# Optimization experiments

Measured on AMD Instinct MI355X. Metric: run time of the kernel, lower is better.

Reference implementation:

```python
import jax, jax.numpy as jnp
import numpy as np

B, T, H, N = 4, 2048, 1024, 16
DT_MIN, DT_MAX = 1e-3, 1e-1
A_INIT_MIN, A_INIT_MAX = 0.5, 2.0


def _inv_softplus(x):
    # log(exp(x) - 1), numerically stable
    return x + jnp.log(-jnp.expm1(-x))


def setup_inputs() -> dict:
    key = jax.random.key(0)
    kx, ka, kb, kc, kw, kdt = jax.random.split(key, 6)
    x = jax.random.normal(kx, (B, T, H), dtype=jnp.float32)
    A_log = jax.random.uniform(ka, (H, N), minval=np.log(A_INIT_MIN), maxval=np.log(A_INIT_MAX), dtype=jnp.float32)
    B_mat = 0.02 * jax.random.normal(kb, (H, N), dtype=jnp.float32)
    C_mat = 0.02 * jax.random.normal(kc, (H, N), dtype=jnp.float32)
    D_vec = jnp.ones((H,), dtype=jnp.float32)
    W_dt = 0.02 * jax.random.normal(kw, (H, H), dtype=jnp.float32)
    b_dt = _inv_softplus(jax.random.uniform(kdt, (H,), minval=DT_MIN, maxval=DT_MAX, dtype=jnp.float32))
    return {"x": x, "A_log": A_log, "B_mat": B_mat, "C_mat": C_mat, "D_vec": D_vec, "W_dt": W_dt, "b_dt": b_dt}


def reference(x, A_log, B_mat, C_mat, D_vec, W_dt, b_dt):
    # in_proj is Identity since input_size == hidden_size
    u = x  # (B, T, H)
    A = -jnp.exp(A_log)  # (H, N)
    # dt for all timesteps at once: softplus(u @ W_dt^T + b_dt) -> (B, T, H)
    dt = jax.nn.softplus(jnp.einsum('bth,gh->btg', u, W_dt) + b_dt)
    state0 = jnp.zeros((u.shape[0], A_log.shape[0], A_log.shape[1]), dtype=u.dtype)

    def step(state, inp):
        dt_t, u_t = inp  # (B, H), (B, H)
        dtA = dt_t[..., None]  # (B, H, 1)
        A_bar = jnp.exp(dtA * A)                       # (B, H, N)
        state = A_bar * state + (dtA * B_mat) * u_t[..., None]
        y_t = jnp.einsum('bhn,hn->bh', state, C_mat) + D_vec * u_t
        return state, y_t

    # scan over time axis
    state_final, ys = jax.lax.scan(step, state0, (dt.transpose(1, 0, 2), u.transpose(1, 0, 2)))
    out = ys.transpose(1, 0, 2)  # (B, T, H)
    return out, state_final
```

## Files before the change

kernel.cpp:

```cpp
#include <hip/hip_runtime.h>
#include <stdint.h>

#define BB 4
#define TT 2048
#define HH 1024
#define NN 16
#define KK 1024
#define GG 1024
#define MM (BB*TT)
#define NCHUNK 64
#define TC (TT/NCHUNK)
#define HB 256

#if __has_builtin(__builtin_amdgcn_exp2f)
#define FAST_EXP2(x) __builtin_amdgcn_exp2f(x)
#else
#define FAST_EXP2(x) __expf((x) * 0.6931471805599453f)
#endif
#define EXPSCALE 1.4426950408889634f

typedef __attribute__((ext_vector_type(8))) short short8;
typedef __attribute__((ext_vector_type(4))) float f32x4;

__device__ __forceinline__ unsigned short f2bf(float f) {
  union { float f; unsigned u; } a; a.f = f;
  unsigned u = a.u;
  u += 0x7fffu + ((u >> 16) & 1u);
  return (unsigned short)(u >> 16);
}

__global__ __launch_bounds__(256) void cvt_f32_bf16(const float* __restrict__ src,
                                                    unsigned short* __restrict__ dst, int n4) {
  int i = blockIdx.x * blockDim.x + threadIdx.x;
  if (i >= n4) return;
  float4 a = ((const float4*)src)[i];
  ushort4 o;
  o.x = f2bf(a.x); o.y = f2bf(a.y); o.z = f2bf(a.z); o.w = f2bf(a.w);
  ((ushort4*)dst)[i] = o;
}

__global__ __launch_bounds__(256) void gemm_dt(const unsigned short* __restrict__ xb,
                                               const unsigned short* __restrict__ wb,
                                               const float* __restrict__ b_dt,
                                               float* __restrict__ dtT) {
  __shared__ short lsA[128 * 32];
  __shared__ short lsB[64 * 32];
  const int tid  = threadIdx.x;
  const int w    = tid >> 6;
  const int lane = tid & 63;
  const int m0 = blockIdx.x * 128;
  const int g0 = blockIdx.y * 64;

  const int ea  = w * 1024 + lane * 8;
  const int am0 = ea >> 5,         ak0 = ea & 31;
  const int am1 = (ea + 512) >> 5, ak1 = (ea + 512) & 31;
  const int eb  = w * 512 + lane * 8;
  const int bg0 = eb >> 5,         bk0 = eb & 31;
  const unsigned short* gA0 = xb + (size_t)(m0 + am0) * KK + ak0;
  const unsigned short* gA1 = xb + (size_t)(m0 + am1) * KK + ak1;
  const unsigned short* gB0 = wb + (size_t)(g0 + bg0) * KK + bk0;
  short* lA0 = lsA + w * 1024;
  short* lB0 = lsB + w * 512;

  const int wm   = (w >> 1) * 64;
  const int wg   = (w & 1) * 32;
  const int lrow = lane & 15;
  const int lq   = lane >> 4;

  f32x4 acc[4][2];
  const f32x4 zero = {0.f, 0.f, 0.f, 0.f};
#pragma unroll
  for (int i = 0; i < 4; ++i)
#pragma unroll
    for (int j = 0; j < 2; ++j) acc[i][j] = zero;

  for (int kt = 0; kt < KK / 32; ++kt) {
    const int ko = kt * 32;
    __builtin_amdgcn_global_load_lds((__attribute__((address_space(1))) void*)(gA0 + ko),
                                     (__attribute__((address_space(3))) void*)(lA0), 16, 0, 0);
    __builtin_amdgcn_global_load_lds((__attribute__((address_space(1))) void*)(gA1 + ko),
                                     (__attribute__((address_space(3))) void*)(lA0 + 512), 16, 0, 0);
    __builtin_amdgcn_global_load_lds((__attribute__((address_space(1))) void*)(gB0 + ko),
                                     (__attribute__((address_space(3))) void*)(lB0), 16, 0, 0);
    __syncthreads();

    short8 af[4], bfr[2];
#pragma unroll
    for (int mi = 0; mi < 4; ++mi)
      af[mi] = *(const short8*)&lsA[(wm + mi * 16 + lrow) * 32 + lq * 8];
#pragma unroll
    for (int ni = 0; ni < 2; ++ni)
      bfr[ni] = *(const short8*)&lsB[(wg + ni * 16 + lrow) * 32 + lq * 8];
#pragma unroll
    for (int mi = 0; mi < 4; ++mi)
#pragma unroll
      for (int ni = 0; ni < 2; ++ni)
        acc[mi][ni] = __builtin_amdgcn_mfma_f32_16x16x32_bf16(af[mi], bfr[ni], acc[mi][ni], 0, 0, 0);
    __syncthreads();
  }

  const int b  = m0 >> 11;
  const int tb = (m0 & (TT - 1)) + wm + lq * 4;
#pragma unroll
  for (int mi = 0; mi < 4; ++mi)
#pragma unroll
    for (int ni = 0; ni < 2; ++ni) {
      const int gcol = g0 + wg + ni * 16 + lrow;
      const float bias = b_dt[gcol];
      f32x4 sp;
#pragma unroll
      for (int r = 0; r < 4; ++r) {
        float z = acc[mi][ni][r] + bias;
        sp[r] = fmaxf(z, 0.f) + __logf(1.f + __expf(-fabsf(z)));
      }
      *(f32x4*)&dtT[((size_t)b * HH + gcol) * TT + tb + mi * 16] = sp;
    }
}

__global__ __launch_bounds__(256, 4) void ssm_phase1(const float* __restrict__ x,
                                                     const float* __restrict__ dtT,
                                                     const float* __restrict__ A_log,
                                                     float* __restrict__ sloc,
                                                     float* __restrict__ sdArr) {
  __shared__ float uT[TC][HB];
  const int tid = threadIdx.x;
  const int bid = blockIdx.x;
  const int hb = bid & (HH / HB - 1);
  const int b  = (bid >> 2) & (BB - 1);
  const int c  = bid >> 4;
  const int h  = hb * HB + tid;

  const float* xg = x + (size_t)b * TT * HH + (size_t)c * TC * HH + hb * HB;
#pragma unroll
  for (int i = 0; i < 8; ++i) {
    const int t   = i * 4 + (tid >> 6);
    const int col = (tid & 63) * 4;
    *(f32x4*)&uT[t][col] = *(const f32x4*)&xg[(size_t)t * HH + col];
  }

  const float* dp = dtT + ((size_t)b * HH + h) * TT + c * TC;
  f32x4 dd[8];
#pragma unroll
  for (int i = 0; i < 8; ++i) dd[i] = ((const f32x4*)dp)[i];

  float Ae[NN];
#pragma unroll
  for (int n = 0; n < NN; ++n) Ae[n] = -__expf(A_log[h * NN + n]) * EXPSCALE;

  float s[NN];
#pragma unroll
  for (int n = 0; n < NN; ++n) s[n] = 0.f;
  float sd = 0.f;

  __syncthreads();

#pragma unroll
  for (int jt = 0; jt < 8; ++jt) {
#pragma unroll
    for (int k = 0; k < 4; ++k) {
      const int t = jt * 4 + k;
      const float dtv = dd[jt][k];
      const float du  = dtv * uT[t][tid];
      sd += dtv;
#pragma unroll
      for (int n = 0; n < NN; ++n) {
        const float ab = FAST_EXP2(dtv * Ae[n]);
        s[n] = fmaf(ab, s[n], du);
      }
    }
  }

  float* sp = sloc + (((size_t)c * BB + b) * HH + h) * NN;
#pragma unroll
  for (int n = 0; n < NN; n += 4) {
    f32x4 v = {s[n], s[n + 1], s[n + 2], s[n + 3]};
    *(f32x4*)&sp[n] = v;
  }
  sdArr[((size_t)c * BB + b) * HH + h] = sd;
}

__global__ __launch_bounds__(256) void ssm_phase2(float* __restrict__ sloc,
                                                  const float* __restrict__ sdArr,
                                                  const float* __restrict__ A_log,
                                                  const float* __restrict__ Bm_,
                                                  float* __restrict__ stateOut) {
  const int id = blockIdx.x * 256 + threadIdx.x;
  const int hn = id & (HH * NN - 1);
  const int bh = id >> 4;
  const float Ae = -__expf(A_log[hn]) * EXPSCALE;
  float carry = 0.f;
  for (int ch = 0; ch < NCHUNK; ++ch) {
    const size_t idx = (size_t)ch * (BB * HH * NN) + id;
    const float sl = sloc[idx];
    const float dc = FAST_EXP2(Ae * sdArr[(size_t)ch * (BB * HH) + bh]);
    sloc[idx] = carry;
    carry = fmaf(dc, carry, sl);
  }
  stateOut[id] = Bm_[hn] * carry;
}

__global__ __launch_bounds__(256, 4) void ssm_phase3(const float* __restrict__ x,
                                                     const float* __restrict__ dtT,
                                                     const float* __restrict__ A_log,
                                                     const float* __restrict__ Bm_,
                                                     const float* __restrict__ Cm_,
                                                     const float* __restrict__ Dv_,
                                                     const float* __restrict__ carryBuf,
                                                     float* __restrict__ out) {
  __shared__ float uT[TC][HB];
  const int tid = threadIdx.x;
  const int bid = blockIdx.x;
  const int hb = bid & (HH / HB - 1);
  const int b  = (bid >> 2) & (BB - 1);
  const int c  = bid >> 4;
  const int h  = hb * HB + tid;

  const float* xg = x + (size_t)b * TT * HH + (size_t)c * TC * HH + hb * HB;
#pragma unroll
  for (int i = 0; i < 8; ++i) {
    const int t   = i * 4 + (tid >> 6);
    const int col = (tid & 63) * 4;
    *(f32x4*)&uT[t][col] = *(const f32x4*)&xg[(size_t)t * HH + col];
  }

  const float* dp = dtT + ((size_t)b * HH + h) * TT + c * TC;
  f32x4 dd[8];
#pragma unroll
  for (int i = 0; i < 8; ++i) dd[i] = ((const f32x4*)dp)[i];

  float Ae[NN], Cb[NN];
#pragma unroll
  for (int n = 0; n < NN; ++n) {
    Ae[n] = -__expf(A_log[h * NN + n]) * EXPSCALE;
    Cb[n] = Cm_[h * NN + n] * Bm_[h * NN + n];
  }
  const float Dv = Dv_[h];

  float s[NN];
  const float* cp = carryBuf + (((size_t)c * BB + b) * HH + h) * NN;
#pragma unroll
  for (int n = 0; n < NN; n += 4) {
    f32x4 v = *(const f32x4*)&cp[n];
    s[n] = v[0]; s[n + 1] = v[1]; s[n + 2] = v[2]; s[n + 3] = v[3];
  }

  float* yo = out + (size_t)b * TT * HH + (size_t)c * TC * HH + h;

  __syncthreads();

#pragma unroll
  for (int jt = 0; jt < 8; ++jt) {
#pragma unroll
    for (int k = 0; k < 4; ++k) {
      const int t = jt * 4 + k;
      const float dtv = dd[jt][k];
      const float uv  = uT[t][tid];
      const float du  = dtv * uv;
      float y = Dv * uv;
#pragma unroll
      for (int n = 0; n < NN; ++n) {
        const float ab = FAST_EXP2(dtv * Ae[n]);
        s[n] = fmaf(ab, s[n], du);
        y = fmaf(Cb[n], s[n], y);
      }
      yo[(size_t)t * HH] = y;
    }
  }
}

extern "C" void kernel_launch(void* const* d_in, const int* in_sizes, int n_in,
                              void* d_out, int out_size, void* d_ws, size_t ws_size,
                              hipStream_t stream) {
  const float* x     = (const float*)d_in[0];
  const float* A_log = (const float*)d_in[1];
  const float* B_mat = (const float*)d_in[2];
  const float* C_mat = (const float*)d_in[3];
  const float* D_vec = (const float*)d_in[4];
  const float* W_dt  = (const float*)d_in[5];
  const float* b_dt  = (const float*)d_in[6];
  float* out = (float*)d_out;

  char* ws = (char*)d_ws;
  unsigned short* xb  = (unsigned short*)(ws);
  unsigned short* wb  = (unsigned short*)(ws + 16777216);
  float*          dtT = (float*)(ws + 18874368);
  float*          sloc  = (float*)(ws);
  float*          sdArr = (float*)(ws + 16777216);
  float* stateOut = out + (size_t)BB * TT * HH;

  cvt_f32_bf16<<<(MM * KK / 4 + 255) / 256, 256, 0, stream>>>(x, xb, MM * KK / 4);
  cvt_f32_bf16<<<(GG * KK / 4 + 255) / 256, 256, 0, stream>>>(W_dt, wb, GG * KK / 4);
  gemm_dt<<<dim3(MM / 128, GG / 64), 256, 0, stream>>>(xb, wb, b_dt, dtT);

  const int nblk = (HH / HB) * BB * NCHUNK;
  ssm_phase1<<<nblk, 256, 0, stream>>>(x, dtT, A_log, sloc, sdArr);
  ssm_phase2<<<(BB * HH * NN) / 256, 256, 0, stream>>>(sloc, sdArr, A_log, B_mat, stateOut);
  ssm_phase3<<<nblk, 256, 0, stream>>>(x, dtT, A_log, B_mat, C_mat, D_vec, sloc, out);
}
```

Before: 184.9 us.

## Store dt in fp16, merge conversion launches, use direct-to-LDS loads and split accumulators

The dt intermediate is now written by the GEMM epilogue as fp16 instead of fp32, halving its write and its two reads in the scan phases. The two bf16 conversion launches are merged into one kernel. The x tile is staged into LDS with global_load_lds instead of going through registers. Phase 3 splits the y reduction across four accumulators to shorten the dependency chain, and phase 2 unrolls its chunk loop. fp16 dt loses precision compared with fp32, which feeds directly into the exponent of the decay.

```diff
diff --git a/kernel.cpp b/kernel.cpp
--- a/kernel.cpp
+++ b/kernel.cpp
@@ -21,6 +21,8 @@
 
 typedef __attribute__((ext_vector_type(8))) short short8;
 typedef __attribute__((ext_vector_type(4))) float f32x4;
+typedef __attribute__((ext_vector_type(8))) _Float16 half8;
+typedef __attribute__((ext_vector_type(4))) _Float16 half4;
 
 __device__ __forceinline__ unsigned short f2bf(float f) {
   union { float f; unsigned u; } a; a.f = f;
@@ -29,20 +31,24 @@
   return (unsigned short)(u >> 16);
 }
 
-__global__ __launch_bounds__(256) void cvt_f32_bf16(const float* __restrict__ src,
-                                                    unsigned short* __restrict__ dst, int n4) {
+__global__ __launch_bounds__(256) void cvt2_f32_bf16(const float* __restrict__ srcA,
+                                                     unsigned short* __restrict__ dstA, int n4a,
+                                                     const float* __restrict__ srcB,
+                                                     unsigned short* __restrict__ dstB, int n4b) {
   int i = blockIdx.x * blockDim.x + threadIdx.x;
-  if (i >= n4) return;
-  float4 a = ((const float4*)src)[i];
+  const float* s; unsigned short* d; int j;
+  if (i < n4a) { s = srcA; d = dstA; j = i; }
+  else         { s = srcB; d = dstB; j = i - n4a; if (j >= n4b) return; }
+  float4 a = ((const float4*)s)[j];
   ushort4 o;
   o.x = f2bf(a.x); o.y = f2bf(a.y); o.z = f2bf(a.z); o.w = f2bf(a.w);
-  ((ushort4*)dst)[i] = o;
+  ((ushort4*)d)[j] = o;
 }
 
 __global__ __launch_bounds__(256) void gemm_dt(const unsigned short* __restrict__ xb,
                                                const unsigned short* __restrict__ wb,
                                                const float* __restrict__ b_dt,
-                                               float* __restrict__ dtT) {
+                                               _Float16* __restrict__ dtH) {
   __shared__ short lsA[128 * 32];
   __shared__ short lsB[64 * 32];
   const int tid  = threadIdx.x;
@@ -107,18 +113,18 @@
     for (int ni = 0; ni < 2; ++ni) {
       const int gcol = g0 + wg + ni * 16 + lrow;
       const float bias = b_dt[gcol];
-      f32x4 sp;
+      half4 sp;
 #pragma unroll
       for (int r = 0; r < 4; ++r) {
         float z = acc[mi][ni][r] + bias;
-        sp[r] = fmaxf(z, 0.f) + __logf(1.f + __expf(-fabsf(z)));
+        sp[r] = (_Float16)(fmaxf(z, 0.f) + __logf(1.f + __expf(-fabsf(z))));
       }
-      *(f32x4*)&dtT[((size_t)b * HH + gcol) * TT + tb + mi * 16] = sp;
+      *(half4*)&dtH[((size_t)b * HH + gcol) * TT + tb + mi * 16] = sp;
     }
 }
 
 __global__ __launch_bounds__(256, 4) void ssm_phase1(const float* __restrict__ x,
-                                                     const float* __restrict__ dtT,
+                                                     const _Float16* __restrict__ dtH,
                                                      const float* __restrict__ A_log,
                                                      float* __restrict__ sloc,
                                                      float* __restrict__ sdArr) {
@@ -129,19 +135,27 @@
   const int b  = (bid >> 2) & (BB - 1);
   const int c  = bid >> 4;
   const int h  = hb * HB + tid;
+  const int w    = tid >> 6;
+  const int lane = tid & 63;
 
   const float* xg = x + (size_t)b * TT * HH + (size_t)c * TC * HH + hb * HB;
 #pragma unroll
   for (int i = 0; i < 8; ++i) {
-    const int t   = i * 4 + (tid >> 6);
-    const int col = (tid & 63) * 4;
-    *(f32x4*)&uT[t][col] = *(const f32x4*)&xg[(size_t)t * HH + col];
-  }
-
-  const float* dp = dtT + ((size_t)b * HH + h) * TT + c * TC;
+    const int t = i * 4 + w;
+    __builtin_amdgcn_global_load_lds(
+        (__attribute__((address_space(1))) void*)(xg + (size_t)t * HH + lane * 4),
+        (__attribute__((address_space(3))) void*)&uT[t][0], 16, 0, 0);
+  }
+
+  const _Float16* dp = dtH + ((size_t)b * HH + h) * TT + c * TC;
+  half8 hv[4];
+#pragma unroll
+  for (int i = 0; i < 4; ++i) hv[i] = ((const half8*)dp)[i];
   f32x4 dd[8];
 #pragma unroll
-  for (int i = 0; i < 8; ++i) dd[i] = ((const f32x4*)dp)[i];
+  for (int i = 0; i < 8; ++i)
+#pragma unroll
+    for (int k = 0; k < 4; ++k) dd[i][k] = (float)hv[i >> 1][(i & 1) * 4 + k];
 
   float Ae[NN];
 #pragma unroll
@@ -189,6 +203,7 @@
   const int bh = id >> 4;
   const float Ae = -__expf(A_log[hn]) * EXPSCALE;
   float carry = 0.f;
+#pragma unroll 4
   for (int ch = 0; ch < NCHUNK; ++ch) {
     const size_t idx = (size_t)ch * (BB * HH * NN) + id;
     const float sl = sloc[idx];
@@ -200,7 +215,7 @@
 }
 
 __global__ __launch_bounds__(256, 4) void ssm_phase3(const float* __restrict__ x,
-                                                     const float* __restrict__ dtT,
+                                                     const _Float16* __restrict__ dtH,
                                                      const float* __restrict__ A_log,
                                                      const float* __restrict__ Bm_,
                                                      const float* __restrict__ Cm_,
@@ -214,19 +229,27 @@
   const int b  = (bid >> 2) & (BB - 1);
   const int c  = bid >> 4;
   const int h  = hb * HB + tid;
+  const int w    = tid >> 6;
+  const int lane = tid & 63;
 
   const float* xg = x + (size_t)b * TT * HH + (size_t)c * TC * HH + hb * HB;
 #pragma unroll
   for (int i = 0; i < 8; ++i) {
-    const int t   = i * 4 + (tid >> 6);
-    const int col = (tid & 63) * 4;
-    *(f32x4*)&uT[t][col] = *(const f32x4*)&xg[(size_t)t * HH + col];
-  }
-
-  const float* dp = dtT + ((size_t)b * HH + h) * TT + c * TC;
+    const int t = i * 4 + w;
+    __builtin_amdgcn_global_load_lds(
+        (__attribute__((address_space(1))) void*)(xg + (size_t)t * HH + lane * 4),
+        (__attribute__((address_space(3))) void*)&uT[t][0], 16, 0, 0);
+  }
+
+  const _Float16* dp = dtH + ((size_t)b * HH + h) * TT + c * TC;
+  half8 hv[4];
+#pragma unroll
+  for (int i = 0; i < 4; ++i) hv[i] = ((const half8*)dp)[i];
   f32x4 dd[8];
 #pragma unroll
-  for (int i = 0; i < 8; ++i) dd[i] = ((const f32x4*)dp)[i];
+  for (int i = 0; i < 8; ++i)
+#pragma unroll
+    for (int k = 0; k < 4; ++k) dd[i][k] = (float)hv[i >> 1][(i & 1) * 4 + k];
 
   float Ae[NN], Cb[NN];
 #pragma unroll
@@ -256,14 +279,16 @@
       const float dtv = dd[jt][k];
       const float uv  = uT[t][tid];
       const float du  = dtv * uv;
-      float y = Dv * uv;
-#pragma unroll
-      for (int n = 0; n < NN; ++n) {
-        const float ab = FAST_EXP2(dtv * Ae[n]);
-        s[n] = fmaf(ab, s[n], du);
-        y = fmaf(Cb[n], s[n], y);
+      float y0 = Dv * uv, y1 = 0.f, y2 = 0.f, y3 = 0.f;
+#pragma unroll
+      for (int n = 0; n < NN; n += 4) {
+        float ab;
+        ab = FAST_EXP2(dtv * Ae[n]);     s[n]     = fmaf(ab, s[n],     du); y0 = fmaf(Cb[n],     s[n],     y0);
+        ab = FAST_EXP2(dtv * Ae[n + 1]); s[n + 1] = fmaf(ab, s[n + 1], du); y1 = fmaf(Cb[n + 1], s[n + 1], y1);
+        ab = FAST_EXP2(dtv * Ae[n + 2]); s[n + 2] = fmaf(ab, s[n + 2], du); y2 = fmaf(Cb[n + 2], s[n + 2], y2);
+        ab = FAST_EXP2(dtv * Ae[n + 3]); s[n + 3] = fmaf(ab, s[n + 3], du); y3 = fmaf(Cb[n + 3], s[n + 3], y3);
       }
-      yo[(size_t)t * HH] = y;
+      yo[(size_t)t * HH] = (y0 + y1) + (y2 + y3);
     }
   }
 }
@@ -283,17 +308,17 @@
   char* ws = (char*)d_ws;
   unsigned short* xb  = (unsigned short*)(ws);
   unsigned short* wb  = (unsigned short*)(ws + 16777216);
-  float*          dtT = (float*)(ws + 18874368);
+  _Float16*       dtH = (_Float16*)(ws + 18874368);
   float*          sloc  = (float*)(ws);
   float*          sdArr = (float*)(ws + 16777216);
   float* stateOut = out + (size_t)BB * TT * HH;
 
-  cvt_f32_bf16<<<(MM * KK / 4 + 255) / 256, 256, 0, stream>>>(x, xb, MM * KK / 4);
-  cvt_f32_bf16<<<(GG * KK / 4 + 255) / 256, 256, 0, stream>>>(W_dt, wb, GG * KK / 4);
-  gemm_dt<<<dim3(MM / 128, GG / 64), 256, 0, stream>>>(xb, wb, b_dt, dtT);
+  const int n4x = MM * KK / 4, n4w = GG * KK / 4;
+  cvt2_f32_bf16<<<(n4x + n4w + 255) / 256, 256, 0, stream>>>(x, xb, n4x, W_dt, wb, n4w);
+  gemm_dt<<<dim3(MM / 128, GG / 64), 256, 0, stream>>>(xb, wb, b_dt, dtH);
 
   const int nblk = (HH / HB) * BB * NCHUNK;
-  ssm_phase1<<<nblk, 256, 0, stream>>>(x, dtT, A_log, sloc, sdArr);
+  ssm_phase1<<<nblk, 256, 0, stream>>>(x, dtH, A_log, sloc, sdArr);
   ssm_phase2<<<(BB * HH * NN) / 256, 256, 0, stream>>>(sloc, sdArr, A_log, B_mat, stateOut);
-  ssm_phase3<<<nblk, 256, 0, stream>>>(x, dtT, A_log, B_mat, C_mat, D_vec, sloc, out);
-}
+  ssm_phase3<<<nblk, 256, 0, stream>>>(x, dtH, A_log, B_mat, C_mat, D_vec, sloc, out);
+}
```

Result: no change. 187.8 us (+1.6%).
